# Performance work log

Measured on AMD Instinct MI355X. Metric: run time of the kernel, lower is better.

Reference implementation:

```python
import jax, jax.numpy as jnp
import numpy as np

N0, R, ND = 500000, 100000, 50000
E0, E1 = 2000000, 1000000
NODE_DIM, REVIEW_DIM, FINAL_DIM, H = 64, 64, 32, 4


def setup_inputs() -> dict:
    key = jax.random.key(0)
    ks = jax.random.split(key, 12)
    x = jax.random.normal(ks[0], (N0, NODE_DIM), dtype=jnp.float32)
    norm_n = jax.random.uniform(ks[1], (N0,), dtype=jnp.float32)
    norm_e = jax.random.uniform(ks[2], (E0,), dtype=jnp.float32)
    W1 = jax.random.normal(ks[3], (NODE_DIM, REVIEW_DIM), dtype=jnp.float32) * 0.05
    b1 = jax.random.normal(ks[4], (REVIEW_DIM,), dtype=jnp.float32) * 0.05
    Wsrc = jax.random.normal(ks[5], (REVIEW_DIM, H * FINAL_DIM), dtype=jnp.float32) * 0.05
    bsrc = jax.random.normal(ks[6], (H * FINAL_DIM,), dtype=jnp.float32) * 0.05
    attn = jax.random.normal(ks[7], (H, FINAL_DIM), dtype=jnp.float32) * 0.05
    src0 = jax.random.randint(ks[8], (E0,), 0, N0, dtype=jnp.int32)
    dst0 = jax.random.randint(ks[9], (E0,), 0, N0, dtype=jnp.int32)
    # 5 nodes per review graph (batched-graph membership for dgl.mean_nodes)
    node_graph = (jnp.arange(N0, dtype=jnp.int32) // (N0 // R)).astype(jnp.int32)
    src1 = jax.random.randint(ks[10], (E1,), 0, R, dtype=jnp.int32)
    dst1 = jax.random.randint(ks[11], (E1,), 0, ND, dtype=jnp.int32)
    # guarantee every dst node has at least one incoming edge (no 0-in-degree)
    dst1 = dst1.at[:ND].set(jnp.arange(ND, dtype=jnp.int32))
    return {"x": x, "norm_n": norm_n, "norm_e": norm_e, "W1": W1, "b1": b1,
            "Wsrc": Wsrc, "bsrc": bsrc, "attn": attn,
            "src0": src0, "dst0": dst0, "node_graph": node_graph,
            "src1": src1, "dst1": dst1}


def _leaky(v, slope):
    return jnp.where(v >= 0, v, slope * v)


def _edge_softmax(score, dst, n):
    # numerically stable per-destination softmax over edges; score [E,H]
    m = jax.ops.segment_max(score, dst, num_segments=n)
    ex = jnp.exp(score - m[dst])
    s = jax.ops.segment_sum(ex, dst, num_segments=n)
    return ex / s[dst]


def reference(x, norm_n, norm_e, W1, b1, Wsrc, bsrc, attn,
              src0, dst0, node_graph, src1, dst1):
    # ---- HypergraphLayer (blocks[0]) ----
    coef = norm_n[src0] * norm_n[dst0] * norm_e            # [E0]
    m = x[src0] * coef[:, None]                            # [E0, D_in]
    h = jax.ops.segment_sum(m, dst0, num_segments=N0)      # [N0, D_in]
    cnt = jax.ops.segment_sum(jnp.ones((N0,), x.dtype), node_graph, num_segments=R)
    r = jax.ops.segment_sum(h, node_graph, num_segments=R) / cnt[:, None]  # mean_nodes -> [R, D_in]
    r = _leaky(r @ W1 + b1, 0.01)                          # [R, review_dim]
    # ---- HEARConv / GATv2 (blocks[1]); fc_dst frozen at zero => er = 0 ----
    feat_src = (r @ Wsrc + bsrc).reshape(R, H, FINAL_DIM)  # [R, H, D]
    el = feat_src[src1]                                    # [E1, H, D]
    e = _leaky(el, 0.2)
    score = jnp.einsum('ehd,hd->eh', e, attn)              # [E1, H]
    alpha = _edge_softmax(score, dst1, ND)                 # [E1, H]
    ft = jax.ops.segment_sum(el * alpha[..., None], dst1, num_segments=ND)  # [ND, H, D]
    return ft.sum(axis=1)                                  # [ND, final_dim]
```

## Files before the change

### kernel.cpp

```cpp
#include <hip/hip_runtime.h>
#include <math.h>

#define N0c 500000
#define Rc  100000
#define NDc 50000
#define E0c 2000000
#define E1c 1000000
#define GB0 64
#define NB0 1563
#define DB1 64
#define NB1 782
#define NBk (NB0 + NB1)
#define T0  3072
#define T1  1536
#define PB  652
#define CAP0 1792
#define CAP1 1792
#define MTILE 32


__global__ __launch_bounds__(1024) void k_place(
        const int* __restrict__ src0, const int* __restrict__ dst0,
        const float* __restrict__ norm_n, const float* __restrict__ norm_e,
        const int* __restrict__ src1, const int* __restrict__ dst1,
        unsigned* __restrict__ gcur,
        int2* __restrict__ coarse0, int* __restrict__ coarse1) {
    __shared__ unsigned cnt_s[NBk];
    __shared__ unsigned lo_s[NBk + 1];
    __shared__ unsigned dst_s[NBk];
    __shared__ unsigned pack_e[T0 + T1];
    __shared__ unsigned pack_s[T0 + T1];
    __shared__ float    pc_s[T0];

    int tid = threadIdx.x, b = blockIdx.x;
    int base0 = b * T0, base1 = b * T1;

    for (int i = tid; i < NBk; i += 1024) cnt_s[i] = 0u;
    __syncthreads();

    for (int i = tid; i < T0; i += 1024) {
        int e = base0 + i;
        if (e < E0c) {
            int d = dst0[e];
            unsigned q5 = (unsigned)d / 5u;
            unsigned bk = q5 >> 6;
            atomicAdd(&cnt_s[bk], 1u);
            pack_e[i] = (unsigned)i | ((q5 & 63u) << 12) | (bk << 18);
            pc_s[i] = norm_n[d] * norm_e[e];
        }
    }
    for (int i = tid; i < T1; i += 1024) {
        int e = base1 + i;
        if (e < E1c) {
            int d = dst1[e];
            unsigned bkAll = NB0 + ((unsigned)d >> 6);
            atomicAdd(&cnt_s[bkAll], 1u);
            pack_e[T0 + i] = (unsigned)i | ((unsigned)(d & 63) << 12) | (bkAll << 18);
        }
    }
    __syncthreads();

    unsigned a0 = (3 * tid     < NBk) ? cnt_s[3 * tid]     : 0u;
    unsigned a1 = (3 * tid + 1 < NBk) ? cnt_s[3 * tid + 1] : 0u;
    unsigned a2 = (3 * tid + 2 < NBk) ? cnt_s[3 * tid + 2] : 0u;
    unsigned ssum = a0 + a1 + a2;
    unsigned* scratch = pack_s;
    scratch[tid] = ssum;
    __syncthreads();
    for (int off = 1; off < 1024; off <<= 1) {
        unsigned t = (tid >= off) ? scratch[tid - off] : 0u;
        __syncthreads();
        scratch[tid] += t;
        __syncthreads();
    }
    unsigned ex = scratch[tid] - ssum;
    if (3 * tid     < NBk) lo_s[3 * tid]     = ex;
    if (3 * tid + 1 < NBk) lo_s[3 * tid + 1] = ex + a0;
    if (3 * tid + 2 < NBk) lo_s[3 * tid + 2] = ex + a0 + a1;
    if (tid == 1023) lo_s[NBk] = scratch[1023];
    __syncthreads();

    for (int i = tid; i < NBk; i += 1024) {
        unsigned c = cnt_s[i];
        unsigned rb = c ? atomicAdd(&gcur[i], c) : 0u;
        unsigned sb = (i < NB0) ? (unsigned)i * CAP0 : (unsigned)(i - NB0) * CAP1;
        dst_s[i] = sb + rb - lo_s[i];
    }
    __syncthreads();
    for (int i = tid; i < NBk; i += 1024) cnt_s[i] = lo_s[i];
    __syncthreads();

    for (int i = tid; i < T0; i += 1024) {
        if (base0 + i < E0c) {
            unsigned pk = pack_e[i];
            unsigned slot = atomicAdd(&cnt_s[pk >> 18], 1u);
            pack_s[slot] = pk;
        }
    }
    for (int i = tid; i < T1; i += 1024) {
        if (base1 + i < E1c) {
            unsigned pk = pack_e[T0 + i];
            unsigned slot = atomicAdd(&cnt_s[pk >> 18], 1u);
            pack_s[slot] = pk;
        }
    }
    __syncthreads();

    unsigned ntot = lo_s[NBk];
    for (unsigned j = tid; j < ntot; j += 1024) {
        unsigned pk = pack_s[j];
        unsigned bkAll = pk >> 18;
        unsigned low = (pk >> 12) & 63u;
        unsigned i = pk & 4095u;
        unsigned idx = dst_s[bkAll] + j;
        if (bkAll < NB0) {
            if (idx - bkAll * CAP0 < CAP0) {
                int e = base0 + (int)i;
                int s = src0[e];
                float coef = pc_s[i] * norm_n[s];
                coarse0[idx] = make_int2(s | (int)(low << 19), __float_as_int(coef));
            }
        } else {
            if (idx - (bkAll - NB0) * CAP1 < CAP1) {
                int e = base1 + (int)i;
                coarse1[idx] = src1[e] | (int)(low << 17);
            }
        }
    }
}

__global__ __launch_bounds__(512) void k_bucket0(
        const float* __restrict__ x, const int2* __restrict__ coarse0,
        const unsigned* __restrict__ gcur, float* __restrict__ r_mean) {
    __shared__ unsigned cur_s[GB0];
    __shared__ unsigned off_s[GB0 + 1];
    __shared__ int2  raw_s[CAP0];
    __shared__ int   sa[CAP0];
    __shared__ float ca[CAP0];
    int B = blockIdx.x, tid = threadIdx.x;
    int g0 = B * GB0;
    int ng = min(GB0, Rc - g0);
    size_t beg = (size_t)B * CAP0;
    int n = min((int)gcur[B], CAP0);
    if (tid < GB0) cur_s[tid] = 0u;
    __syncthreads();
    for (int i = tid; i < n; i += 512) {
        int2 p = coarse0[beg + i];
        raw_s[i] = p;
        atomicAdd(&cur_s[(p.x >> 19) & 63], 1u);
    }
    __syncthreads();
    if (tid < 64) {
        unsigned c = cur_s[tid];
        unsigned sc = c;
        for (int o = 1; o < 64; o <<= 1) {
            unsigned t = __shfl_up(sc, o);
            if (tid >= o) sc += t;
        }
        off_s[tid] = sc - c;
        if (tid == 63) off_s[GB0] = sc;
    }
    __syncthreads();
    if (tid < GB0) cur_s[tid] = off_s[tid];
    __syncthreads();
    for (int i = tid; i < n; i += 512) {
        int2 p = raw_s[i];
        unsigned slot = atomicAdd(&cur_s[(p.x >> 19) & 63], 1u);
        sa[slot] = p.x & 0x7FFFF;
        ca[slot] = __int_as_float(p.y);
    }
    __syncthreads();
    int wav = tid >> 6, lane = tid & 63, q = lane >> 4, l = lane & 15;
    for (int g = wav; g < ng; g += 8) {
        int rbeg = (int)off_s[g], rend = (int)off_s[g + 1];
        float4 acc = {0.f, 0.f, 0.f, 0.f};
        for (int j0 = rbeg + q; j0 < rend; j0 += 16) {
            int j1 = j0 + 4, j2 = j0 + 8, j3 = j0 + 12;
            int s0 = sa[j0];                 float c0 = ca[j0];
            int s1 = 0; float c1 = 0.f;
            int s2 = 0; float c2 = 0.f;
            int s3 = 0; float c3 = 0.f;
            if (j1 < rend) { s1 = sa[j1]; c1 = ca[j1]; }
            if (j2 < rend) { s2 = sa[j2]; c2 = ca[j2]; }
            if (j3 < rend) { s3 = sa[j3]; c3 = ca[j3]; }
            float4 v0 = ((const float4*)(x + (size_t)s0 * 64))[l];
            float4 v1 = ((const float4*)(x + (size_t)s1 * 64))[l];
            float4 v2 = ((const float4*)(x + (size_t)s2 * 64))[l];
            float4 v3 = ((const float4*)(x + (size_t)s3 * 64))[l];
            acc.x += v0.x * c0 + v1.x * c1 + v2.x * c2 + v3.x * c3;
            acc.y += v0.y * c0 + v1.y * c1 + v2.y * c2 + v3.y * c3;
            acc.z += v0.z * c0 + v1.z * c1 + v2.z * c2 + v3.z * c3;
            acc.w += v0.w * c0 + v1.w * c1 + v2.w * c2 + v3.w * c3;
        }
        acc.x += __shfl_xor(acc.x, 16); acc.y += __shfl_xor(acc.y, 16);
        acc.z += __shfl_xor(acc.z, 16); acc.w += __shfl_xor(acc.w, 16);
        acc.x += __shfl_xor(acc.x, 32); acc.y += __shfl_xor(acc.y, 32);
        acc.z += __shfl_xor(acc.z, 32); acc.w += __shfl_xor(acc.w, 32);
        if (q == 0) {
            float4 o = {acc.x * 0.2f, acc.y * 0.2f, acc.z * 0.2f, acc.w * 0.2f};
            ((float4*)(r_mean + (size_t)(g0 + g) * 64))[l] = o;
        }
    }
}

__global__ __launch_bounds__(512) void k_mlp(const float* __restrict__ r_in,
                                             const float* __restrict__ W1,
                                             const float* __restrict__ b1,
                                             const float* __restrict__ Wsrc,
                                             const float* __restrict__ bsrc,
                                             const float* __restrict__ attn,
                                             float* __restrict__ feat,
                                             float* __restrict__ score_src, int R) {
    __shared__ float W1s[64 * 64];
    __shared__ float Wss[64 * 128];
    __shared__ float b1s[64], bss[128], atts[128];
    __shared__ float in_s[MTILE * 68];
    __shared__ float t1_s[MTILE * 68];
    int tid = threadIdx.x;
    for (int i = tid; i < 4096; i += 512) W1s[i] = W1[i];
    for (int i = tid; i < 8192; i += 512) Wss[i] = Wsrc[i];
    if (tid < 64) b1s[tid] = b1[tid];
    if (tid >= 64 && tid < 192) bss[tid - 64] = bsrc[tid - 64];
    if (tid >= 192 && tid < 320) atts[tid - 192] = attn[tid - 192];

    int row = tid >> 4, c = tid & 15;
    size_t grow = (size_t)blockIdx.x * MTILE + row;
    float4 vin = ((const float4*)(r_in + grow * 64))[c];
    *((float4*)&in_s[row * 68 + c * 4]) = vin;
    __syncthreads();

    {
        float4 a = {0.f, 0.f, 0.f, 0.f};
        const float* wcol = W1s + c * 4;
        const float* inr = in_s + row * 68;
#pragma unroll
        for (int k = 0; k < 64; k++) {
            float iv = inr[k];
            float4 w = *((const float4*)(wcol + k * 64));
            a.x += iv * w.x; a.y += iv * w.y;
            a.z += iv * w.z; a.w += iv * w.w;
        }
        const float4 bb = *((const float4*)(b1s + c * 4));
        a.x += bb.x; a.y += bb.y; a.z += bb.z; a.w += bb.w;
        a.x = a.x >= 0.f ? a.x : 0.01f * a.x;
        a.y = a.y >= 0.f ? a.y : 0.01f * a.y;
        a.z = a.z >= 0.f ? a.z : 0.01f * a.z;
        a.w = a.w >= 0.f ? a.w : 0.01f * a.w;
        *((float4*)&t1_s[row * 68 + c * 4]) = a;
    }
    __syncthreads();

    {
        float4 a0 = {0.f, 0.f, 0.f, 0.f}, a1 = {0.f, 0.f, 0.f, 0.f};
        const float* w2 = Wss + c * 8;
        const float* t1r = t1_s + row * 68;
#pragma unroll
        for (int k = 0; k < 64; k++) {
            float tv = t1r[k];
            float4 w0 = *((const float4*)(w2 + k * 128));
            float4 w1 = *((const float4*)(w2 + k * 128 + 4));
            a0.x += tv * w0.x; a0.y += tv * w0.y;
            a0.z += tv * w0.z; a0.w += tv * w0.w;
            a1.x += tv * w1.x; a1.y += tv * w1.y;
            a1.z += tv * w1.z; a1.w += tv * w1.w;
        }
        const float4 b0 = *((const float4*)(bss + c * 8));
        const float4 b1v = *((const float4*)(bss + c * 8 + 4));
        a0.x += b0.x; a0.y += b0.y; a0.z += b0.z; a0.w += b0.w;
        a1.x += b1v.x; a1.y += b1v.y; a1.z += b1v.z; a1.w += b1v.w;
        float4* fp = (float4*)(feat + grow * 128 + c * 8);
        fp[0] = a0; fp[1] = a1;
        const float4 at0 = *((const float4*)(atts + c * 8));
        const float4 at1 = *((const float4*)(atts + c * 8 + 4));
        float p =
            (a0.x >= 0.f ? a0.x : 0.2f * a0.x) * at0.x +
            (a0.y >= 0.f ? a0.y : 0.2f * a0.y) * at0.y +
            (a0.z >= 0.f ? a0.z : 0.2f * a0.z) * at0.z +
            (a0.w >= 0.f ? a0.w : 0.2f * a0.w) * at0.w +
            (a1.x >= 0.f ? a1.x : 0.2f * a1.x) * at1.x +
            (a1.y >= 0.f ? a1.y : 0.2f * a1.y) * at1.y +
            (a1.z >= 0.f ? a1.z : 0.2f * a1.z) * at1.z +
            (a1.w >= 0.f ? a1.w : 0.2f * a1.w) * at1.w;
        p += __shfl_xor(p, 1);
        p += __shfl_xor(p, 2);
        if ((c & 3) == 0) score_src[grow * 4 + (c >> 2)] = p;
    }
}

__global__ __launch_bounds__(512) void k_bucket1(
        const float* __restrict__ feat, const float* __restrict__ score,
        const int* __restrict__ coarse1, const unsigned* __restrict__ gcur,
        float* __restrict__ out) {
    __shared__ unsigned cur_s[DB1];
    __shared__ unsigned off_s[DB1 + 1];
    __shared__ int raw_s[CAP1];
    __shared__ int sa[CAP1];
    int B = blockIdx.x, tid = threadIdx.x;
    int d0 = B * DB1;
    int nd = min(DB1, NDc - d0);
    size_t beg = (size_t)B * CAP1;
    int n = min((int)gcur[NB0 + B], CAP1);
    if (tid < DB1) cur_s[tid] = 0u;
    __syncthreads();
    for (int i = tid; i < n; i += 512) {
        int p = coarse1[beg + i];
        raw_s[i] = p;
        atomicAdd(&cur_s[(p >> 17) & 63], 1u);
    }
    __syncthreads();
    if (tid < 64) {
        unsigned c = cur_s[tid];
        unsigned sc = c;
        for (int o = 1; o < 64; o <<= 1) {
            unsigned t = __shfl_up(sc, o);
            if (tid >= o) sc += t;
        }
        off_s[tid] = sc - c;
        if (tid == 63) off_s[DB1] = sc;
    }
    __syncthreads();
    if (tid < DB1) cur_s[tid] = off_s[tid];
    __syncthreads();
    for (int i = tid; i < n; i += 512) {
        int p = raw_s[i];
        unsigned slot = atomicAdd(&cur_s[(p >> 17) & 63], 1u);
        sa[slot] = p & 0x1FFFF;
    }
    __syncthreads();
    int wav = tid >> 6, lane = tid & 63, q = lane >> 5, l = lane & 31, h = l >> 3;
    const float NEG = -3.0e38f;
    for (int dl = wav; dl < nd; dl += 8) {
        int rbeg = (int)off_s[dl], rend = (int)off_s[dl + 1];
        float4 mx = {NEG, NEG, NEG, NEG};
        for (int j = rbeg + lane; j < rend; j += 64) {
            int s = sa[j];
            float4 sc = ((const float4*)score)[s];
            mx.x = fmaxf(mx.x, sc.x); mx.y = fmaxf(mx.y, sc.y);
            mx.z = fmaxf(mx.z, sc.z); mx.w = fmaxf(mx.w, sc.w);
        }
#pragma unroll
        for (int o = 1; o < 64; o <<= 1) {
            mx.x = fmaxf(mx.x, __shfl_xor(mx.x, o));
            mx.y = fmaxf(mx.y, __shfl_xor(mx.y, o));
            mx.z = fmaxf(mx.z, __shfl_xor(mx.z, o));
            mx.w = fmaxf(mx.w, __shfl_xor(mx.w, o));
        }
        float mh = h == 0 ? mx.x : h == 1 ? mx.y : h == 2 ? mx.z : mx.w;
        float4 acc = {0.f, 0.f, 0.f, 0.f};
        float sex = 0.f;
        for (int j0 = rbeg + q; j0 < rend; j0 += 8) {
            int j1 = j0 + 2, j2 = j0 + 4, j3 = j0 + 6;
            int s0 = sa[j0];
            bool v1 = j1 < rend, v2 = j2 < rend, v3 = j3 < rend;
            int s1 = v1 ? sa[j1] : s0;
            int s2 = v2 ? sa[j2] : s0;
            int s3 = v3 ? sa[j3] : s0;
            float sc0 = score[4 * s0 + h];
            float sc1 = score[4 * s1 + h];
            float sc2 = score[4 * s2 + h];
            float sc3 = score[4 * s3 + h];
            float4 f0 = ((const float4*)(feat + (size_t)s0 * 128))[l];
            float4 f1 = ((const float4*)(feat + (size_t)s1 * 128))[l];
            float4 f2 = ((const float4*)(feat + (size_t)s2 * 128))[l];
            float4 f3 = ((const float4*)(feat + (size_t)s3 * 128))[l];
            float e0 = __expf(sc0 - mh);
            float e1 = v1 ? __expf(sc1 - mh) : 0.f;
            float e2 = v2 ? __expf(sc2 - mh) : 0.f;
            float e3 = v3 ? __expf(sc3 - mh) : 0.f;
            acc.x += f0.x * e0 + f1.x * e1 + f2.x * e2 + f3.x * e3;
            acc.y += f0.y * e0 + f1.y * e1 + f2.y * e2 + f3.y * e3;
            acc.z += f0.z * e0 + f1.z * e1 + f2.z * e2 + f3.z * e3;
            acc.w += f0.w * e0 + f1.w * e1 + f2.w * e2 + f3.w * e3;
            sex += e0 + e1 + e2 + e3;
        }
        acc.x += __shfl_xor(acc.x, 32); acc.y += __shfl_xor(acc.y, 32);
        acc.z += __shfl_xor(acc.z, 32); acc.w += __shfl_xor(acc.w, 32);
        sex += __shfl_xor(sex, 32);
        float inv = 1.f / sex;
        acc.x *= inv; acc.y *= inv; acc.z *= inv; acc.w *= inv;
        acc.x += __shfl_xor(acc.x, 8);  acc.y += __shfl_xor(acc.y, 8);
        acc.z += __shfl_xor(acc.z, 8);  acc.w += __shfl_xor(acc.w, 8);
        acc.x += __shfl_xor(acc.x, 16); acc.y += __shfl_xor(acc.y, 16);
        acc.z += __shfl_xor(acc.z, 16); acc.w += __shfl_xor(acc.w, 16);
        if (lane < 8) ((float4*)(out + (size_t)(d0 + dl) * 32))[lane] = acc;
    }
}

extern "C" void kernel_launch(void* const* d_in, const int* in_sizes, int n_in,
                              void* d_out, int out_size, void* d_ws, size_t ws_size,
                              hipStream_t stream) {
    const float* x      = (const float*)d_in[0];
    const float* norm_n = (const float*)d_in[1];
    const float* norm_e = (const float*)d_in[2];
    const float* W1     = (const float*)d_in[3];
    const float* b1     = (const float*)d_in[4];
    const float* Wsrc   = (const float*)d_in[5];
    const float* bsrc   = (const float*)d_in[6];
    const float* attn   = (const float*)d_in[7];
    const int* src0     = (const int*)d_in[8];
    const int* dst0     = (const int*)d_in[9];
    const int* src1     = (const int*)d_in[11];
    const int* dst1     = (const int*)d_in[12];
    float* out = (float*)d_out;

    char* ws = (char*)d_ws;
    size_t off = 0;
    auto alloc = [&](size_t bytes) {
        void* p = ws + off;
        off += (bytes + 255) & ~(size_t)255;
        return p;
    };

    unsigned* gcur = (unsigned*)alloc(NBk * 4);
    size_t zero_bytes = off;
    size_t featB = (size_t)Rc * 128 * 4;
    char* pA = (char*)alloc(featB);
    int2* coarse0 = (int2*)pA;
    float* feat   = (float*)pA;
    int* coarse1  = (int*)alloc((size_t)NB1 * CAP1 * 4);
    float* r_mean = (float*)alloc((size_t)Rc * 64 * 4);
    float* score_src = (float*)alloc((size_t)Rc * 4 * 4);

    hipMemsetAsync(d_ws, 0, zero_bytes, stream);

    k_place<<<PB, 1024, 0, stream>>>(src0, dst0, norm_n, norm_e,
                                     src1, dst1, gcur, coarse0, coarse1);

    k_bucket0<<<NB0, 512, 0, stream>>>(x, coarse0, gcur, r_mean);
    k_mlp<<<Rc / MTILE, 512, 0, stream>>>(r_mean, W1, b1, Wsrc, bsrc, attn, feat, score_src, Rc);
    k_bucket1<<<NB1, 512, 0, stream>>>(feat, score_src, coarse1, gcur, out);
}
```

Before: 507.2 us.

## Store gathered node and source features in fp16 to halve gather traffic

A new pre-pass kernel converts the input node features x to fp16 on every call. The first bucket kernel then gathers 128-byte half rows instead of 256-byte float rows. The MLP kernel writes the projected source features as fp16, and the attention aggregation kernel gathers those half rows too, with all accumulation kept in fp32. The aim is to cut the bytes moved by the random per-edge gathers, in exchange for an extra full read/write pass over x and some loss of precision in the features.

```diff
diff --git a/kernel.cpp b/kernel.cpp
--- a/kernel.cpp
+++ b/kernel.cpp
@@ -1,4 +1,5 @@
 #include <hip/hip_runtime.h>
+#include <hip/hip_fp16.h>
 #include <math.h>
 
 #define N0c 500000
@@ -18,6 +19,23 @@
 #define CAP1 1792
 #define MTILE 32
 
+
+__global__ __launch_bounds__(256) void k_convert(const float4* __restrict__ x,
+                                                 uint4* __restrict__ xh) {
+    int i = blockIdx.x * 256 + threadIdx.x;
+    const int NT = (N0c * 64) / 8;
+    if (i < NT) {
+        float4 a = x[2 * i], b = x[2 * i + 1];
+        __half2 h0 = __floats2half2_rn(a.x, a.y);
+        __half2 h1 = __floats2half2_rn(a.z, a.w);
+        __half2 h2 = __floats2half2_rn(b.x, b.y);
+        __half2 h3 = __floats2half2_rn(b.z, b.w);
+        uint4 o;
+        o.x = *(unsigned*)&h0; o.y = *(unsigned*)&h1;
+        o.z = *(unsigned*)&h2; o.w = *(unsigned*)&h3;
+        xh[i] = o;
+    }
+}
 
 __global__ __launch_bounds__(1024) void k_place(
         const int* __restrict__ src0, const int* __restrict__ dst0,
@@ -130,7 +148,7 @@
 }
 
 __global__ __launch_bounds__(512) void k_bucket0(
-        const float* __restrict__ x, const int2* __restrict__ coarse0,
+        const __half* __restrict__ xh, const int2* __restrict__ coarse0,
         const unsigned* __restrict__ gcur, float* __restrict__ r_mean) {
     __shared__ unsigned cur_s[GB0];
     __shared__ unsigned off_s[GB0 + 1];
@@ -183,14 +201,18 @@
             if (j1 < rend) { s1 = sa[j1]; c1 = ca[j1]; }
             if (j2 < rend) { s2 = sa[j2]; c2 = ca[j2]; }
             if (j3 < rend) { s3 = sa[j3]; c3 = ca[j3]; }
-            float4 v0 = ((const float4*)(x + (size_t)s0 * 64))[l];
-            float4 v1 = ((const float4*)(x + (size_t)s1 * 64))[l];
-            float4 v2 = ((const float4*)(x + (size_t)s2 * 64))[l];
-            float4 v3 = ((const float4*)(x + (size_t)s3 * 64))[l];
-            acc.x += v0.x * c0 + v1.x * c1 + v2.x * c2 + v3.x * c3;
-            acc.y += v0.y * c0 + v1.y * c1 + v2.y * c2 + v3.y * c3;
-            acc.z += v0.z * c0 + v1.z * c1 + v2.z * c2 + v3.z * c3;
-            acc.w += v0.w * c0 + v1.w * c1 + v2.w * c2 + v3.w * c3;
+            uint2 u0 = ((const uint2*)(xh + (size_t)s0 * 64))[l];
+            uint2 u1 = ((const uint2*)(xh + (size_t)s1 * 64))[l];
+            uint2 u2 = ((const uint2*)(xh + (size_t)s2 * 64))[l];
+            uint2 u3 = ((const uint2*)(xh + (size_t)s3 * 64))[l];
+            float2 a0 = __half22float2(*(__half2*)&u0.x), b0 = __half22float2(*(__half2*)&u0.y);
+            float2 a1 = __half22float2(*(__half2*)&u1.x), b1 = __half22float2(*(__half2*)&u1.y);
+            float2 a2 = __half22float2(*(__half2*)&u2.x), b2 = __half22float2(*(__half2*)&u2.y);
+            float2 a3 = __half22float2(*(__half2*)&u3.x), b3 = __half22float2(*(__half2*)&u3.y);
+            acc.x += a0.x * c0 + a1.x * c1 + a2.x * c2 + a3.x * c3;
+            acc.y += a0.y * c0 + a1.y * c1 + a2.y * c2 + a3.y * c3;
+            acc.z += b0.x * c0 + b1.x * c1 + b2.x * c2 + b3.x * c3;
+            acc.w += b0.y * c0 + b1.y * c1 + b2.y * c2 + b3.y * c3;
         }
         acc.x += __shfl_xor(acc.x, 16); acc.y += __shfl_xor(acc.y, 16);
         acc.z += __shfl_xor(acc.z, 16); acc.w += __shfl_xor(acc.w, 16);
@@ -209,7 +231,7 @@
                                              const float* __restrict__ Wsrc,
                                              const float* __restrict__ bsrc,
                                              const float* __restrict__ attn,
-                                             float* __restrict__ feat,
+                                             __half* __restrict__ feat_h,
                                              float* __restrict__ score_src, int R) {
     __shared__ float W1s[64 * 64];
     __shared__ float Wss[64 * 128];
@@ -268,8 +290,14 @@
         const float4 b1v = *((const float4*)(bss + c * 8 + 4));
         a0.x += b0.x; a0.y += b0.y; a0.z += b0.z; a0.w += b0.w;
         a1.x += b1v.x; a1.y += b1v.y; a1.z += b1v.z; a1.w += b1v.w;
-        float4* fp = (float4*)(feat + grow * 128 + c * 8);
-        fp[0] = a0; fp[1] = a1;
+        __half2 h0 = __floats2half2_rn(a0.x, a0.y);
+        __half2 h1 = __floats2half2_rn(a0.z, a0.w);
+        __half2 h2 = __floats2half2_rn(a1.x, a1.y);
+        __half2 h3 = __floats2half2_rn(a1.z, a1.w);
+        uint4 w;
+        w.x = *(unsigned*)&h0; w.y = *(unsigned*)&h1;
+        w.z = *(unsigned*)&h2; w.w = *(unsigned*)&h3;
+        *(uint4*)(feat_h + grow * 128 + c * 8) = w;
         const float4 at0 = *((const float4*)(atts + c * 8));
         const float4 at1 = *((const float4*)(atts + c * 8 + 4));
         float p =
@@ -288,7 +316,7 @@
 }
 
 __global__ __launch_bounds__(512) void k_bucket1(
-        const float* __restrict__ feat, const float* __restrict__ score,
+        const __half* __restrict__ feat_h, const float* __restrict__ score,
         const int* __restrict__ coarse1, const unsigned* __restrict__ gcur,
         float* __restrict__ out) {
     __shared__ unsigned cur_s[DB1];
@@ -359,18 +387,22 @@
             float sc1 = score[4 * s1 + h];
             float sc2 = score[4 * s2 + h];
             float sc3 = score[4 * s3 + h];
-            float4 f0 = ((const float4*)(feat + (size_t)s0 * 128))[l];
-            float4 f1 = ((const float4*)(feat + (size_t)s1 * 128))[l];
-            float4 f2 = ((const float4*)(feat + (size_t)s2 * 128))[l];
-            float4 f3 = ((const float4*)(feat + (size_t)s3 * 128))[l];
+            uint2 u0 = ((const uint2*)(feat_h + (size_t)s0 * 128))[l];
+            uint2 u1 = ((const uint2*)(feat_h + (size_t)s1 * 128))[l];
+            uint2 u2 = ((const uint2*)(feat_h + (size_t)s2 * 128))[l];
+            uint2 u3 = ((const uint2*)(feat_h + (size_t)s3 * 128))[l];
             float e0 = __expf(sc0 - mh);
             float e1 = v1 ? __expf(sc1 - mh) : 0.f;
             float e2 = v2 ? __expf(sc2 - mh) : 0.f;
             float e3 = v3 ? __expf(sc3 - mh) : 0.f;
-            acc.x += f0.x * e0 + f1.x * e1 + f2.x * e2 + f3.x * e3;
-            acc.y += f0.y * e0 + f1.y * e1 + f2.y * e2 + f3.y * e3;
-            acc.z += f0.z * e0 + f1.z * e1 + f2.z * e2 + f3.z * e3;
-            acc.w += f0.w * e0 + f1.w * e1 + f2.w * e2 + f3.w * e3;
+            float2 f0a = __half22float2(*(__half2*)&u0.x), f0b = __half22float2(*(__half2*)&u0.y);
+            float2 f1a = __half22float2(*(__half2*)&u1.x), f1b = __half22float2(*(__half2*)&u1.y);
+            float2 f2a = __half22float2(*(__half2*)&u2.x), f2b = __half22float2(*(__half2*)&u2.y);
+            float2 f3a = __half22float2(*(__half2*)&u3.x), f3b = __half22float2(*(__half2*)&u3.y);
+            acc.x += f0a.x * e0 + f1a.x * e1 + f2a.x * e2 + f3a.x * e3;
+            acc.y += f0a.y * e0 + f1a.y * e1 + f2a.y * e2 + f3a.y * e3;
+            acc.z += f0b.x * e0 + f1b.x * e1 + f2b.x * e2 + f3b.x * e3;
+            acc.w += f0b.y * e0 + f1b.y * e1 + f2b.y * e2 + f3b.y * e3;
             sex += e0 + e1 + e2 + e3;
         }
         acc.x += __shfl_xor(acc.x, 32); acc.y += __shfl_xor(acc.y, 32);
@@ -413,20 +445,22 @@
 
     unsigned* gcur = (unsigned*)alloc(NBk * 4);
     size_t zero_bytes = off;
-    size_t featB = (size_t)Rc * 128 * 4;
-    char* pA = (char*)alloc(featB);
-    int2* coarse0 = (int2*)pA;
-    float* feat   = (float*)pA;
+    __half* xh = (__half*)alloc((size_t)N0c * 64 * 2);
+    size_t regA = (size_t)Rc * 128 * 2;
+    char* pA = (char*)alloc(regA);
+    int2* coarse0  = (int2*)pA;
+    __half* feat_h = (__half*)pA;
     int* coarse1  = (int*)alloc((size_t)NB1 * CAP1 * 4);
     float* r_mean = (float*)alloc((size_t)Rc * 64 * 4);
     float* score_src = (float*)alloc((size_t)Rc * 4 * 4);
 
     hipMemsetAsync(d_ws, 0, zero_bytes, stream);
 
+    k_convert<<<(N0c * 64 / 8 + 255) / 256, 256, 0, stream>>>((const float4*)x, (uint4*)xh);
     k_place<<<PB, 1024, 0, stream>>>(src0, dst0, norm_n, norm_e,
                                      src1, dst1, gcur, coarse0, coarse1);
 
-    k_bucket0<<<NB0, 512, 0, stream>>>(x, coarse0, gcur, r_mean);
-    k_mlp<<<Rc / MTILE, 512, 0, stream>>>(r_mean, W1, b1, Wsrc, bsrc, attn, feat, score_src, Rc);
-    k_bucket1<<<NB1, 512, 0, stream>>>(feat, score_src, coarse1, gcur, out);
-}
+    k_bucket0<<<NB0, 512, 0, stream>>>(xh, coarse0, gcur, r_mean);
+    k_mlp<<<Rc / MTILE, 512, 0, stream>>>(r_mean, W1, b1, Wsrc, bsrc, attn, feat_h, score_src, Rc);
+    k_bucket1<<<NB1, 512, 0, stream>>>(feat_h, score_src, coarse1, gcur, out);
+}
```

New measurement: 474.5 us. 1.07x faster.
